# Optimization experiments

Hardware: AMD Instinct MI355X
Metric: run time of the kernel (lower is better)

The kernel has to match this reference:

```python
import jax, jax.numpy as jnp
import numpy as np

N_SPECIES = 2
N_RBF = 16
HIDDEN = 64
CUTOFF = 2.5


def setup_inputs() -> dict:
    key = jax.random.key(0)
    ks = jax.random.split(key, 10)
    B, N = 8, 1024
    positions = jax.random.uniform(ks[0], (B, N, 3), dtype=jnp.float32) * 10.0
    types = jax.random.randint(ks[1], (B, N), 0, N_SPECIES)
    in_dim = N_SPECIES + N_SPECIES * N_RBF  # 34
    def lin(k, fan_in, fan_out):
        bound = 1.0 / np.sqrt(fan_in)
        kw, kb = jax.random.split(k)
        W = jax.random.uniform(kw, (fan_in, fan_out), minval=-bound, maxval=bound, dtype=jnp.float32)
        b = jax.random.uniform(kb, (fan_out,), minval=-bound, maxval=bound, dtype=jnp.float32)
        return W, b
    W1, b1 = lin(ks[2], in_dim, 64)
    W2, b2 = lin(ks[3], 64, 64)
    W3, b3 = lin(ks[4], 64, HIDDEN)
    return {"positions": positions, "types": types,
            "W1": W1, "b1": b1, "W2": W2, "b2": b2, "W3": W3, "b3": b3}


def _forward(positions, types, W1, b1, W2, b2, W3, b3):
    B, N, _ = positions.shape
    # pairwise distances with safe sqrt (zero grad on diagonal, matching torch norm subgradient)
    disp = positions[:, :, None, :] - positions[:, None, :, :]          # [B,N,N,3]
    sq = jnp.sum(disp * disp, axis=-1)                                   # [B,N,N]
    nz = sq > 0.0
    d = jnp.sqrt(jnp.where(nz, sq, 1.0)) * nz
    # RBF expansion
    centers = jnp.linspace(0.0, CUTOFF, N_RBF)
    widths = jnp.full((N_RBF,), CUTOFF / max(N_RBF - 1, 1))
    diff = d[..., None] - centers                                        # [B,N,N,R]
    rbf = jnp.exp(-(diff ** 2) / (widths ** 2 + 1e-12))
    # smooth polynomial cutoff
    x = d / CUTOFF
    cut = jnp.where(d < CUTOFF, 1.0 - 6.0 * x ** 5 + 15.0 * x ** 4 - 10.0 * x ** 3, 0.0)
    rbf = rbf * cut[..., None]
    eye = jnp.eye(N, dtype=bool)[None, :, :, None]
    rbf = jnp.where(eye, 0.0, rbf)
    # species-weighted neighbor aggregation
    onehot = jax.nn.one_hot(types, N_SPECIES, dtype=positions.dtype)      # [B,N,S]
    env = jnp.einsum('bijr,bjs->birs', rbf, onehot).reshape(B, N, -1)     # [B,N,R*S]
    feats = jnp.concatenate([onehot, env], axis=-1)                       # [B,N,S+S*R]
    h = jax.nn.silu(feats @ W1 + b1)
    h = jax.nn.silu(h @ W2 + b2)
    return h @ W3 + b3                                                    # [B,N,HIDDEN]


def reference(positions, types, W1, b1, W2, b2, W3, b3):
    return _forward(positions, types, W1, b1, W2, b2, W3, b3)
```

## Files before the change

kernel.cpp:

```cpp
#include <hip/hip_runtime.h>

#define NTHREADS 256
#define N_ATOMS 1024
#define HIDDEN 64

__global__ __launch_bounds__(NTHREADS) void LocalFeatureEncoder_40063454937486_kernel(
    const float* __restrict__ pos,
    const int*   __restrict__ types,
    const float* __restrict__ W1,
    const float* __restrict__ b1,
    const float* __restrict__ W2,
    const float* __restrict__ b2,
    const float* __restrict__ W3,
    const float* __restrict__ b3,
    float*       __restrict__ out)
{
    const int a    = blockIdx.x;
    const int bidx = a >> 10;
    const int i    = a & (N_ATOMS - 1);
    const int tid  = threadIdx.x;
    const int lane = tid & 63;
    const int wav  = tid >> 6;

    __shared__ float qd [N_ATOMS];
    __shared__ float qm [N_ATOMS];
    __shared__ float partial[4 * 32];
    __shared__ float feats[64];
    __shared__ float h1s[64];
    __shared__ int   cnt;

    const float* pf   = pos + (size_t)bidx * (N_ATOMS * 3);
    const int*   typb = types + (size_t)bidx * N_ATOMS;

    const float4 p0 = *(const float4*)(pf + tid * 12);
    const float4 p1 = *(const float4*)(pf + tid * 12 + 4);
    const float4 p2 = *(const float4*)(pf + tid * 12 + 8);
    const int4   tv = *(const int4*)(typb + tid * 4);

    const float xi = pf[i * 3 + 0];
    const float yi = pf[i * 3 + 1];
    const float zi = pf[i * 3 + 2];

    if (tid == 0) cnt = 0;
    __syncthreads();

    {
        const float px[4] = {p0.x, p0.w, p1.z, p2.y};
        const float py[4] = {p0.y, p1.x, p1.w, p2.z};
        const float pz[4] = {p0.z, p1.y, p2.x, p2.w};
        const int   tj[4] = {tv.x, tv.y, tv.z, tv.w};

        float sq[4];
        bool  pr[4];
        unsigned long long m[4];
#pragma unroll
        for (int q = 0; q < 4; ++q) {
            const int j = tid * 4 + q;
            const float dx = xi - px[q], dy = yi - py[q], dz = zi - pz[q];
            sq[q] = dx * dx + dy * dy + dz * dz;
            pr[q] = (j != i) && (sq[q] < 6.25f);
            m[q]  = __ballot(pr[q]);
        }

        const int tot = (int)(__popcll(m[0]) + __popcll(m[1]) +
                              __popcll(m[2]) + __popcll(m[3]));
        int base = 0;
        if (lane == 0 && tot) base = atomicAdd(&cnt, tot);
        base = __shfl(base, 0, 64);

        const unsigned long long lt = (1ull << lane) - 1ull;
        int off = base;
#pragma unroll
        for (int q = 0; q < 4; ++q) {
            if (pr[q]) {
                const float d  = sqrtf(sq[q]);
                const float x  = d * 0.4f;
                const float x3 = x * x * x;
                const float cutv = 1.0f + x3 * (-10.0f + x * (15.0f - 6.0f * x));
                const int idx = off + (int)__popcll(m[q] & lt);
                qd[idx] = d;
                qm[idx] = (tj[q] == 0) ? cutv : -cutv;
            }
            off += (int)__popcll(m[q]);
        }
    }
    __syncthreads();
    const int n = cnt;

    {
        const int slot = tid >> 4;
        const int r    = tid & 15;
        const float c  = (float)r * (2.5f / 15.0f);

        float a0 = 0.0f, a1 = 0.0f;
        for (int e = slot; e < n; e += 16) {
            const float d    = qd[e];
            const float mm   = qm[e];
            const float diff = d - c;
            const float ex   = __expf(-(diff * diff) * 36.0f);
            a0 = fmaf(fmaxf( mm, 0.0f), ex, a0);
            a1 = fmaf(fmaxf(-mm, 0.0f), ex, a1);
        }
        a0 += __shfl_xor(a0, 16, 64);  a0 += __shfl_xor(a0, 32, 64);
        a1 += __shfl_xor(a1, 16, 64);  a1 += __shfl_xor(a1, 32, 64);
        if (lane < 16) {
            partial[wav * 32 + 2 * r]     = a0;
            partial[wav * 32 + 2 * r + 1] = a1;
        }
        if (tid == 0) {
            const int ti = typb[i];
            feats[0] = (ti == 0) ? 1.0f : 0.0f;
            feats[1] = (ti == 1) ? 1.0f : 0.0f;
        }
    }
    __syncthreads();

    if (tid < HIDDEN) {
        if (tid < 32)
            feats[2 + tid] = partial[tid] + partial[32 + tid] +
                             partial[64 + tid] + partial[96 + tid];
        __builtin_amdgcn_wave_barrier();

        float h = b1[tid];
#pragma unroll
        for (int k = 0; k < 34; k++) h = fmaf(feats[k], W1[k * HIDDEN + tid], h);
        h = h / (1.0f + __expf(-h));
        h1s[tid] = h;
        __builtin_amdgcn_wave_barrier();

        float g = b2[tid];
#pragma unroll
        for (int k = 0; k < HIDDEN; k++) g = fmaf(h1s[k], W2[k * HIDDEN + tid], g);
        g = g / (1.0f + __expf(-g));
        feats[tid] = g;
        __builtin_amdgcn_wave_barrier();

        float o = b3[tid];
#pragma unroll
        for (int k = 0; k < HIDDEN; k++) o = fmaf(feats[k], W3[k * HIDDEN + tid], o);
        out[(size_t)a * HIDDEN + tid] = o;
    }
}

extern "C" void kernel_launch(void* const* d_in, const int* in_sizes, int n_in,
                              void* d_out, int out_size, void* d_ws, size_t ws_size,
                              hipStream_t stream) {
    const float* pos   = (const float*)d_in[0];
    const int*   types = (const int*)d_in[1];
    const float* W1    = (const float*)d_in[2];
    const float* b1    = (const float*)d_in[3];
    const float* W2    = (const float*)d_in[4];
    const float* b2    = (const float*)d_in[5];
    const float* W3    = (const float*)d_in[6];
    const float* b3    = (const float*)d_in[7];
    float*       out   = (float*)d_out;

    const int BN = in_sizes[1];

    LocalFeatureEncoder_40063454937486_kernel<<<BN, NTHREADS, 0, stream>>>(
        pos, types, W1, b1, W2, b2, W3, b3, out);
}
```

Measured before the change: 85.12 us.

## Process two atoms per block to amortize position loads and MLP weight reads

Each block now handles two consecutive atoms instead of one, halving the grid. The per-block load of all 1024 positions, the compaction atomics (packed into one 32-bit counter), and the MLP weight reads are shared across both atoms, with the hidden activations interleaved as float2. This trades fewer blocks and doubled LDS use for less redundant global traffic and per-block overhead. The RBF loop now iterates to the larger of the two neighbor counts with branches inside, which can add divergence.

```diff
diff --git a/kernel.cpp b/kernel.cpp
--- a/kernel.cpp
+++ b/kernel.cpp
@@ -15,19 +15,21 @@
     const float* __restrict__ b3,
     float*       __restrict__ out)
 {
-    const int a    = blockIdx.x;
-    const int bidx = a >> 10;
-    const int i    = a & (N_ATOMS - 1);
+    const int blk  = blockIdx.x;
+    const int bidx = blk >> 9;
+    const int i0   = (blk & 511) * 2;
+    const int i1   = i0 + 1;
     const int tid  = threadIdx.x;
     const int lane = tid & 63;
     const int wav  = tid >> 6;
 
-    __shared__ float qd [N_ATOMS];
-    __shared__ float qm [N_ATOMS];
-    __shared__ float partial[4 * 32];
-    __shared__ float feats[64];
-    __shared__ float h1s[64];
-    __shared__ int   cnt;
+    __shared__ __align__(16) float qd[2][N_ATOMS];
+    __shared__ __align__(16) float qm[2][N_ATOMS];
+    __shared__ __align__(16) float partial[4 * 64];
+    __shared__ __align__(16) float feats[34 * 2];
+    __shared__ __align__(16) float h1s[HIDDEN * 2];
+    __shared__ __align__(16) float h2s[HIDDEN * 2];
+    __shared__ int cnt;
 
     const float* pf   = pos + (size_t)bidx * (N_ATOMS * 3);
     const int*   typb = types + (size_t)bidx * N_ATOMS;
@@ -37,9 +39,8 @@
     const float4 p2 = *(const float4*)(pf + tid * 12 + 8);
     const int4   tv = *(const int4*)(typb + tid * 4);
 
-    const float xi = pf[i * 3 + 0];
-    const float yi = pf[i * 3 + 1];
-    const float zi = pf[i * 3 + 2];
+    const float xi0 = pf[i0 * 3 + 0], yi0 = pf[i0 * 3 + 1], zi0 = pf[i0 * 3 + 2];
+    const float xi1 = pf[i1 * 3 + 0], yi1 = pf[i1 * 3 + 1], zi1 = pf[i1 * 3 + 2];
 
     if (tid == 0) cnt = 0;
     __syncthreads();
@@ -50,95 +51,155 @@
         const float pz[4] = {p0.z, p1.y, p2.x, p2.w};
         const int   tj[4] = {tv.x, tv.y, tv.z, tv.w};
 
-        float sq[4];
-        bool  pr[4];
-        unsigned long long m[4];
+        float sq0[4], sq1[4];
+        bool  pr0[4], pr1[4];
+        unsigned long long m0[4], m1[4];
 #pragma unroll
         for (int q = 0; q < 4; ++q) {
             const int j = tid * 4 + q;
-            const float dx = xi - px[q], dy = yi - py[q], dz = zi - pz[q];
-            sq[q] = dx * dx + dy * dy + dz * dz;
-            pr[q] = (j != i) && (sq[q] < 6.25f);
-            m[q]  = __ballot(pr[q]);
-        }
-
-        const int tot = (int)(__popcll(m[0]) + __popcll(m[1]) +
-                              __popcll(m[2]) + __popcll(m[3]));
-        int base = 0;
-        if (lane == 0 && tot) base = atomicAdd(&cnt, tot);
-        base = __shfl(base, 0, 64);
+            float dx = xi0 - px[q], dy = yi0 - py[q], dz = zi0 - pz[q];
+            sq0[q] = dx * dx + dy * dy + dz * dz;
+            dx = xi1 - px[q]; dy = yi1 - py[q]; dz = zi1 - pz[q];
+            sq1[q] = dx * dx + dy * dy + dz * dz;
+            pr0[q] = (j != i0) && (sq0[q] < 6.25f);
+            pr1[q] = (j != i1) && (sq1[q] < 6.25f);
+            m0[q]  = __ballot(pr0[q]);
+            m1[q]  = __ballot(pr1[q]);
+        }
+
+        const int tot0 = (int)(__popcll(m0[0]) + __popcll(m0[1]) +
+                               __popcll(m0[2]) + __popcll(m0[3]));
+        const int tot1 = (int)(__popcll(m1[0]) + __popcll(m1[1]) +
+                               __popcll(m1[2]) + __popcll(m1[3]));
+        int basep = 0;
+        if (lane == 0) basep = atomicAdd(&cnt, tot0 | (tot1 << 16));
+        basep = __shfl(basep, 0, 64);
 
         const unsigned long long lt = (1ull << lane) - 1ull;
-        int off = base;
+        int off0 = basep & 0xffff;
+        int off1 = (basep >> 16) & 0xffff;
 #pragma unroll
         for (int q = 0; q < 4; ++q) {
-            if (pr[q]) {
-                const float d  = sqrtf(sq[q]);
+            if (pr0[q]) {
+                const float d  = sqrtf(sq0[q]);
                 const float x  = d * 0.4f;
                 const float x3 = x * x * x;
                 const float cutv = 1.0f + x3 * (-10.0f + x * (15.0f - 6.0f * x));
-                const int idx = off + (int)__popcll(m[q] & lt);
-                qd[idx] = d;
-                qm[idx] = (tj[q] == 0) ? cutv : -cutv;
-            }
-            off += (int)__popcll(m[q]);
+                const int idx = off0 + (int)__popcll(m0[q] & lt);
+                qd[0][idx] = d;
+                qm[0][idx] = (tj[q] == 0) ? cutv : -cutv;
+            }
+            if (pr1[q]) {
+                const float d  = sqrtf(sq1[q]);
+                const float x  = d * 0.4f;
+                const float x3 = x * x * x;
+                const float cutv = 1.0f + x3 * (-10.0f + x * (15.0f - 6.0f * x));
+                const int idx = off1 + (int)__popcll(m1[q] & lt);
+                qd[1][idx] = d;
+                qm[1][idx] = (tj[q] == 0) ? cutv : -cutv;
+            }
+            off0 += (int)__popcll(m0[q]);
+            off1 += (int)__popcll(m1[q]);
         }
     }
     __syncthreads();
-    const int n = cnt;
+    const int packed = cnt;
+    const int n0   = packed & 0xffff;
+    const int n1   = (packed >> 16) & 0xffff;
+    const int nmax = (n0 > n1) ? n0 : n1;
 
     {
         const int slot = tid >> 4;
         const int r    = tid & 15;
         const float c  = (float)r * (2.5f / 15.0f);
 
-        float a0 = 0.0f, a1 = 0.0f;
-        for (int e = slot; e < n; e += 16) {
-            const float d    = qd[e];
-            const float mm   = qm[e];
-            const float diff = d - c;
-            const float ex   = __expf(-(diff * diff) * 36.0f);
-            a0 = fmaf(fmaxf( mm, 0.0f), ex, a0);
-            a1 = fmaf(fmaxf(-mm, 0.0f), ex, a1);
-        }
-        a0 += __shfl_xor(a0, 16, 64);  a0 += __shfl_xor(a0, 32, 64);
-        a1 += __shfl_xor(a1, 16, 64);  a1 += __shfl_xor(a1, 32, 64);
+        float a00 = 0.0f, a10 = 0.0f;
+        float a01 = 0.0f, a11 = 0.0f;
+        for (int e = slot; e < nmax; e += 16) {
+            if (e < n0) {
+                const float d    = qd[0][e];
+                const float mm   = qm[0][e];
+                const float diff = d - c;
+                const float ex   = __expf(-(diff * diff) * 36.0f);
+                a00 = fmaf(fmaxf( mm, 0.0f), ex, a00);
+                a10 = fmaf(fmaxf(-mm, 0.0f), ex, a10);
+            }
+            if (e < n1) {
+                const float d    = qd[1][e];
+                const float mm   = qm[1][e];
+                const float diff = d - c;
+                const float ex   = __expf(-(diff * diff) * 36.0f);
+                a01 = fmaf(fmaxf( mm, 0.0f), ex, a01);
+                a11 = fmaf(fmaxf(-mm, 0.0f), ex, a11);
+            }
+        }
+        a00 += __shfl_xor(a00, 16, 64);  a00 += __shfl_xor(a00, 32, 64);
+        a10 += __shfl_xor(a10, 16, 64);  a10 += __shfl_xor(a10, 32, 64);
+        a01 += __shfl_xor(a01, 16, 64);  a01 += __shfl_xor(a01, 32, 64);
+        a11 += __shfl_xor(a11, 16, 64);  a11 += __shfl_xor(a11, 32, 64);
         if (lane < 16) {
-            partial[wav * 32 + 2 * r]     = a0;
-            partial[wav * 32 + 2 * r + 1] = a1;
+            const float4 v = {a00, a01, a10, a11};
+            *(float4*)&partial[wav * 64 + r * 4] = v;
         }
         if (tid == 0) {
-            const int ti = typb[i];
-            feats[0] = (ti == 0) ? 1.0f : 0.0f;
-            feats[1] = (ti == 1) ? 1.0f : 0.0f;
+            const int t0 = typb[i0], t1 = typb[i1];
+            feats[0] = (t0 == 0) ? 1.0f : 0.0f;
+            feats[1] = (t1 == 0) ? 1.0f : 0.0f;
+            feats[2] = (t0 == 1) ? 1.0f : 0.0f;
+            feats[3] = (t1 == 1) ? 1.0f : 0.0f;
         }
     }
     __syncthreads();
 
     if (tid < HIDDEN) {
-        if (tid < 32)
-            feats[2 + tid] = partial[tid] + partial[32 + tid] +
-                             partial[64 + tid] + partial[96 + tid];
+        if (tid < 32) {
+            float2 acc      = *(const float2*)&partial[tid * 2];
+            const float2 q1 = *(const float2*)&partial[ 64 + tid * 2];
+            const float2 q2 = *(const float2*)&partial[128 + tid * 2];
+            const float2 q3 = *(const float2*)&partial[192 + tid * 2];
+            acc.x += q1.x + q2.x + q3.x;
+            acc.y += q1.y + q2.y + q3.y;
+            *(float2*)&feats[(2 + tid) * 2] = acc;
+        }
         __builtin_amdgcn_wave_barrier();
 
-        float h = b1[tid];
-#pragma unroll
-        for (int k = 0; k < 34; k++) h = fmaf(feats[k], W1[k * HIDDEN + tid], h);
-        h = h / (1.0f + __expf(-h));
-        h1s[tid] = h;
+        float h0 = b1[tid], h1v = b1[tid];
+#pragma unroll
+        for (int k = 0; k < 34; ++k) {
+            const float w  = W1[k * HIDDEN + tid];
+            const float2 f = *(const float2*)&feats[k * 2];
+            h0  = fmaf(f.x, w, h0);
+            h1v = fmaf(f.y, w, h1v);
+        }
+        h0  = h0  / (1.0f + __expf(-h0));
+        h1v = h1v / (1.0f + __expf(-h1v));
+        *(float2*)&h1s[tid * 2] = make_float2(h0, h1v);
         __builtin_amdgcn_wave_barrier();
 
-        float g = b2[tid];
-#pragma unroll
-        for (int k = 0; k < HIDDEN; k++) g = fmaf(h1s[k], W2[k * HIDDEN + tid], g);
-        g = g / (1.0f + __expf(-g));
-        feats[tid] = g;
+        float g0 = b2[tid], g1 = b2[tid];
+#pragma unroll
+        for (int k = 0; k < HIDDEN; ++k) {
+            const float w  = W2[k * HIDDEN + tid];
+            const float2 f = *(const float2*)&h1s[k * 2];
+            g0 = fmaf(f.x, w, g0);
+            g1 = fmaf(f.y, w, g1);
+        }
+        g0 = g0 / (1.0f + __expf(-g0));
+        g1 = g1 / (1.0f + __expf(-g1));
+        *(float2*)&h2s[tid * 2] = make_float2(g0, g1);
         __builtin_amdgcn_wave_barrier();
 
-        float o = b3[tid];
-#pragma unroll
-        for (int k = 0; k < HIDDEN; k++) o = fmaf(feats[k], W3[k * HIDDEN + tid], o);
-        out[(size_t)a * HIDDEN + tid] = o;
+        float o0 = b3[tid], o1 = b3[tid];
+#pragma unroll
+        for (int k = 0; k < HIDDEN; ++k) {
+            const float w  = W3[k * HIDDEN + tid];
+            const float2 f = *(const float2*)&h2s[k * 2];
+            o0 = fmaf(f.x, w, o0);
+            o1 = fmaf(f.y, w, o1);
+        }
+        const size_t row0 = (size_t)(bidx * N_ATOMS + i0) * HIDDEN;
+        out[row0 + tid]          = o0;
+        out[row0 + HIDDEN + tid] = o1;
     }
 }
 
@@ -156,7 +217,8 @@
     float*       out   = (float*)d_out;
 
     const int BN = in_sizes[1];
-
-    LocalFeatureEncoder_40063454937486_kernel<<<BN, NTHREADS, 0, stream>>>(
+    const int nblocks = BN >> 1;
+
+    LocalFeatureEncoder_40063454937486_kernel<<<nblocks, NTHREADS, 0, stream>>>(
         pos, types, W1, b1, W2, b2, W3, b3, out);
 }
```

After: 84.63 us, median of 2. About the same (-0.6%).

## Process four atoms per block to amortize position loads and MLP weights

Applied to the files above, without the earlier changes.

Each block now handles four center atoms instead of one. The neighbor positions it loads are reused across all four atoms, neighbor counts for pairs of atoms are packed into a single atomic, and the three MLP layers run with four accumulators per weight load. This cuts redundant global loads of positions and weights and lowers the block count by four. In exchange it uses more LDS and registers per block and adds divergence in the RBF loop when the four atoms have different neighbor counts.

```diff
diff --git a/kernel.cpp b/kernel.cpp
--- a/kernel.cpp
+++ b/kernel.cpp
@@ -15,19 +15,21 @@
     const float* __restrict__ b3,
     float*       __restrict__ out)
 {
-    const int a    = blockIdx.x;
-    const int bidx = a >> 10;
-    const int i    = a & (N_ATOMS - 1);
+    const int blk  = blockIdx.x;
+    const int bidx = blk >> 8;
+    const int i0   = (blk & 255) * 4;
     const int tid  = threadIdx.x;
     const int lane = tid & 63;
     const int wav  = tid >> 6;
 
-    __shared__ float qd [N_ATOMS];
-    __shared__ float qm [N_ATOMS];
-    __shared__ float partial[4 * 32];
-    __shared__ float feats[64];
-    __shared__ float h1s[64];
-    __shared__ int   cnt;
+    __shared__ __align__(16) float qd[4][N_ATOMS];
+    __shared__ __align__(16) float qm[4][N_ATOMS];
+    __shared__ __align__(16) float partial[4 * 128];
+    __shared__ __align__(16) float feats[34 * 4];
+    __shared__ __align__(16) float h1s[HIDDEN * 4];
+    __shared__ __align__(16) float h2s[HIDDEN * 4];
+    __shared__ int cnt01;
+    __shared__ int cnt23;
 
     const float* pf   = pos + (size_t)bidx * (N_ATOMS * 3);
     const int*   typb = types + (size_t)bidx * N_ATOMS;
@@ -37,11 +39,15 @@
     const float4 p2 = *(const float4*)(pf + tid * 12 + 8);
     const int4   tv = *(const int4*)(typb + tid * 4);
 
-    const float xi = pf[i * 3 + 0];
-    const float yi = pf[i * 3 + 1];
-    const float zi = pf[i * 3 + 2];
-
-    if (tid == 0) cnt = 0;
+    float xi[4], yi[4], zi[4];
+#pragma unroll
+    for (int a = 0; a < 4; ++a) {
+        xi[a] = pf[(i0 + a) * 3 + 0];
+        yi[a] = pf[(i0 + a) * 3 + 1];
+        zi[a] = pf[(i0 + a) * 3 + 2];
+    }
+
+    if (tid == 0) { cnt01 = 0; cnt23 = 0; }
     __syncthreads();
 
     {
@@ -49,96 +55,181 @@
         const float py[4] = {p0.y, p1.x, p1.w, p2.z};
         const float pz[4] = {p0.z, p1.y, p2.x, p2.w};
         const int   tj[4] = {tv.x, tv.y, tv.z, tv.w};
-
-        float sq[4];
-        bool  pr[4];
-        unsigned long long m[4];
-#pragma unroll
-        for (int q = 0; q < 4; ++q) {
-            const int j = tid * 4 + q;
-            const float dx = xi - px[q], dy = yi - py[q], dz = zi - pz[q];
-            sq[q] = dx * dx + dy * dy + dz * dz;
-            pr[q] = (j != i) && (sq[q] < 6.25f);
-            m[q]  = __ballot(pr[q]);
-        }
-
-        const int tot = (int)(__popcll(m[0]) + __popcll(m[1]) +
-                              __popcll(m[2]) + __popcll(m[3]));
-        int base = 0;
-        if (lane == 0 && tot) base = atomicAdd(&cnt, tot);
-        base = __shfl(base, 0, 64);
-
         const unsigned long long lt = (1ull << lane) - 1ull;
-        int off = base;
-#pragma unroll
-        for (int q = 0; q < 4; ++q) {
-            if (pr[q]) {
-                const float d  = sqrtf(sq[q]);
-                const float x  = d * 0.4f;
-                const float x3 = x * x * x;
-                const float cutv = 1.0f + x3 * (-10.0f + x * (15.0f - 6.0f * x));
-                const int idx = off + (int)__popcll(m[q] & lt);
-                qd[idx] = d;
-                qm[idx] = (tj[q] == 0) ? cutv : -cutv;
-            }
-            off += (int)__popcll(m[q]);
+
+#pragma unroll
+        for (int pass = 0; pass < 2; ++pass) {
+            const int aA = pass * 2, aB = pass * 2 + 1;
+            const int iA = i0 + aA,  iB = i0 + aB;
+            int* cptr = pass ? &cnt23 : &cnt01;
+
+            float sqA[4], sqB[4];
+            bool  prA[4], prB[4];
+            unsigned long long mA[4], mB[4];
+#pragma unroll
+            for (int q = 0; q < 4; ++q) {
+                const int j = tid * 4 + q;
+                float dx = xi[aA] - px[q], dy = yi[aA] - py[q], dz = zi[aA] - pz[q];
+                sqA[q] = dx * dx + dy * dy + dz * dz;
+                dx = xi[aB] - px[q]; dy = yi[aB] - py[q]; dz = zi[aB] - pz[q];
+                sqB[q] = dx * dx + dy * dy + dz * dz;
+                prA[q] = (j != iA) && (sqA[q] < 6.25f);
+                prB[q] = (j != iB) && (sqB[q] < 6.25f);
+                mA[q]  = __ballot(prA[q]);
+                mB[q]  = __ballot(prB[q]);
+            }
+
+            const int totA = (int)(__popcll(mA[0]) + __popcll(mA[1]) +
+                                   __popcll(mA[2]) + __popcll(mA[3]));
+            const int totB = (int)(__popcll(mB[0]) + __popcll(mB[1]) +
+                                   __popcll(mB[2]) + __popcll(mB[3]));
+            int basep = 0;
+            if (lane == 0) basep = atomicAdd(cptr, totA | (totB << 16));
+            basep = __shfl(basep, 0, 64);
+
+            int offA = basep & 0xffff;
+            int offB = (basep >> 16) & 0xffff;
+#pragma unroll
+            for (int q = 0; q < 4; ++q) {
+                if (prA[q]) {
+                    const float d  = sqrtf(sqA[q]);
+                    const float x  = d * 0.4f;
+                    const float x3 = x * x * x;
+                    const float cutv = 1.0f + x3 * (-10.0f + x * (15.0f - 6.0f * x));
+                    const int idx = offA + (int)__popcll(mA[q] & lt);
+                    qd[aA][idx] = d;
+                    qm[aA][idx] = (tj[q] == 0) ? cutv : -cutv;
+                }
+                if (prB[q]) {
+                    const float d  = sqrtf(sqB[q]);
+                    const float x  = d * 0.4f;
+                    const float x3 = x * x * x;
+                    const float cutv = 1.0f + x3 * (-10.0f + x * (15.0f - 6.0f * x));
+                    const int idx = offB + (int)__popcll(mB[q] & lt);
+                    qd[aB][idx] = d;
+                    qm[aB][idx] = (tj[q] == 0) ? cutv : -cutv;
+                }
+                offA += (int)__popcll(mA[q]);
+                offB += (int)__popcll(mB[q]);
+            }
         }
     }
     __syncthreads();
-    const int n = cnt;
+    int n[4];
+    {
+        const int pk01 = cnt01, pk23 = cnt23;
+        n[0] = pk01 & 0xffff;  n[1] = (pk01 >> 16) & 0xffff;
+        n[2] = pk23 & 0xffff;  n[3] = (pk23 >> 16) & 0xffff;
+    }
+    int nmax = n[0];
+    if (n[1] > nmax) nmax = n[1];
+    if (n[2] > nmax) nmax = n[2];
+    if (n[3] > nmax) nmax = n[3];
 
     {
         const int slot = tid >> 4;
         const int r    = tid & 15;
         const float c  = (float)r * (2.5f / 15.0f);
 
-        float a0 = 0.0f, a1 = 0.0f;
-        for (int e = slot; e < n; e += 16) {
-            const float d    = qd[e];
-            const float mm   = qm[e];
-            const float diff = d - c;
-            const float ex   = __expf(-(diff * diff) * 36.0f);
-            a0 = fmaf(fmaxf( mm, 0.0f), ex, a0);
-            a1 = fmaf(fmaxf(-mm, 0.0f), ex, a1);
-        }
-        a0 += __shfl_xor(a0, 16, 64);  a0 += __shfl_xor(a0, 32, 64);
-        a1 += __shfl_xor(a1, 16, 64);  a1 += __shfl_xor(a1, 32, 64);
+        float a0[4] = {0.f, 0.f, 0.f, 0.f};
+        float a1[4] = {0.f, 0.f, 0.f, 0.f};
+        for (int e = slot; e < nmax; e += 16) {
+#pragma unroll
+            for (int a = 0; a < 4; ++a) {
+                if (e < n[a]) {
+                    const float d    = qd[a][e];
+                    const float mm   = qm[a][e];
+                    const float diff = d - c;
+                    const float ex   = __expf(-(diff * diff) * 36.0f);
+                    a0[a] = fmaf(fmaxf( mm, 0.0f), ex, a0[a]);
+                    a1[a] = fmaf(fmaxf(-mm, 0.0f), ex, a1[a]);
+                }
+            }
+        }
+#pragma unroll
+        for (int a = 0; a < 4; ++a) {
+            a0[a] += __shfl_xor(a0[a], 16, 64);  a0[a] += __shfl_xor(a0[a], 32, 64);
+            a1[a] += __shfl_xor(a1[a], 16, 64);  a1[a] += __shfl_xor(a1[a], 32, 64);
+        }
         if (lane < 16) {
-            partial[wav * 32 + 2 * r]     = a0;
-            partial[wav * 32 + 2 * r + 1] = a1;
+            const float4 v0 = {a0[0], a0[1], a0[2], a0[3]};
+            const float4 v1 = {a1[0], a1[1], a1[2], a1[3]};
+            *(float4*)&partial[wav * 128 + r * 8]     = v0;
+            *(float4*)&partial[wav * 128 + r * 8 + 4] = v1;
         }
         if (tid == 0) {
-            const int ti = typb[i];
-            feats[0] = (ti == 0) ? 1.0f : 0.0f;
-            feats[1] = (ti == 1) ? 1.0f : 0.0f;
+#pragma unroll
+            for (int a = 0; a < 4; ++a) {
+                const int t = typb[i0 + a];
+                feats[a]     = (t == 0) ? 1.0f : 0.0f;
+                feats[4 + a] = (t == 1) ? 1.0f : 0.0f;
+            }
         }
     }
     __syncthreads();
 
     if (tid < HIDDEN) {
-        if (tid < 32)
-            feats[2 + tid] = partial[tid] + partial[32 + tid] +
-                             partial[64 + tid] + partial[96 + tid];
+        if (tid < 32) {
+            float4 acc      = *(const float4*)&partial[tid * 4];
+            const float4 q1 = *(const float4*)&partial[128 + tid * 4];
+            const float4 q2 = *(const float4*)&partial[256 + tid * 4];
+            const float4 q3 = *(const float4*)&partial[384 + tid * 4];
+            acc.x += q1.x + q2.x + q3.x;
+            acc.y += q1.y + q2.y + q3.y;
+            acc.z += q1.z + q2.z + q3.z;
+            acc.w += q1.w + q2.w + q3.w;
+            *(float4*)&feats[8 + tid * 4] = acc;
+        }
         __builtin_amdgcn_wave_barrier();
 
-        float h = b1[tid];
-#pragma unroll
-        for (int k = 0; k < 34; k++) h = fmaf(feats[k], W1[k * HIDDEN + tid], h);
-        h = h / (1.0f + __expf(-h));
-        h1s[tid] = h;
+        float h[4];
+        {
+            const float bb = b1[tid];
+            h[0] = bb; h[1] = bb; h[2] = bb; h[3] = bb;
+#pragma unroll
+            for (int k = 0; k < 34; ++k) {
+                const float w  = W1[k * HIDDEN + tid];
+                const float4 f = *(const float4*)&feats[k * 4];
+                h[0] = fmaf(f.x, w, h[0]);  h[1] = fmaf(f.y, w, h[1]);
+                h[2] = fmaf(f.z, w, h[2]);  h[3] = fmaf(f.w, w, h[3]);
+            }
+#pragma unroll
+            for (int a = 0; a < 4; ++a) h[a] = h[a] / (1.0f + __expf(-h[a]));
+            *(float4*)&h1s[tid * 4] = make_float4(h[0], h[1], h[2], h[3]);
+        }
         __builtin_amdgcn_wave_barrier();
 
-        float g = b2[tid];
-#pragma unroll
-        for (int k = 0; k < HIDDEN; k++) g = fmaf(h1s[k], W2[k * HIDDEN + tid], g);
-        g = g / (1.0f + __expf(-g));
-        feats[tid] = g;
+        {
+            const float bb = b2[tid];
+            h[0] = bb; h[1] = bb; h[2] = bb; h[3] = bb;
+#pragma unroll
+            for (int k = 0; k < HIDDEN; ++k) {
+                const float w  = W2[k * HIDDEN + tid];
+                const float4 f = *(const float4*)&h1s[k * 4];
+                h[0] = fmaf(f.x, w, h[0]);  h[1] = fmaf(f.y, w, h[1]);
+                h[2] = fmaf(f.z, w, h[2]);  h[3] = fmaf(f.w, w, h[3]);
+            }
+#pragma unroll
+            for (int a = 0; a < 4; ++a) h[a] = h[a] / (1.0f + __expf(-h[a]));
+            *(float4*)&h2s[tid * 4] = make_float4(h[0], h[1], h[2], h[3]);
+        }
         __builtin_amdgcn_wave_barrier();
 
-        float o = b3[tid];
-#pragma unroll
-        for (int k = 0; k < HIDDEN; k++) o = fmaf(feats[k], W3[k * HIDDEN + tid], o);
-        out[(size_t)a * HIDDEN + tid] = o;
+        {
+            const float bb = b3[tid];
+            float o[4] = {bb, bb, bb, bb};
+#pragma unroll
+            for (int k = 0; k < HIDDEN; ++k) {
+                const float w  = W3[k * HIDDEN + tid];
+                const float4 f = *(const float4*)&h2s[k * 4];
+                o[0] = fmaf(f.x, w, o[0]);  o[1] = fmaf(f.y, w, o[1]);
+                o[2] = fmaf(f.z, w, o[2]);  o[3] = fmaf(f.w, w, o[3]);
+            }
+            const size_t row0 = (size_t)(bidx * N_ATOMS + i0) * HIDDEN;
+#pragma unroll
+            for (int a = 0; a < 4; ++a)
+                out[row0 + (size_t)a * HIDDEN + tid] = o[a];
+        }
     }
 }
 
@@ -156,7 +247,8 @@
     float*       out   = (float*)d_out;
 
     const int BN = in_sizes[1];
-
-    LocalFeatureEncoder_40063454937486_kernel<<<BN, NTHREADS, 0, stream>>>(
+    const int nblocks = BN >> 2;
+
+    LocalFeatureEncoder_40063454937486_kernel<<<nblocks, NTHREADS, 0, stream>>>(
         pos, types, W1, b1, W2, b2, W3, b3, out);
 }
```

Result: slower. 88.82 us (+4.3%).
